# Kernel tuning notes

Hardware: AMD Instinct MI355X
Metric: run time of the kernel (lower is better)

## Reference

```python
import jax, jax.numpy as jnp
import numpy as np

N, K, D = 50000, 16, 128
EPS = 1e-5

def _linear_params(key, fan_in, shape_w, shape_b):
    k1, k2 = jax.random.split(key)
    s = 1.0 / np.sqrt(fan_in)
    W = jax.random.uniform(k1, shape_w, minval=-s, maxval=s, dtype=jnp.float32)
    b = jax.random.uniform(k2, shape_b, minval=-s, maxval=s, dtype=jnp.float32)
    return W, b

def setup_inputs() -> dict:
    key = jax.random.key(0)
    ks = jax.random.split(key, 9)
    Wh, bh = _linear_params(ks[0], D, (D, D), (D,))
    Wt, bt = _linear_params(ks[1], D, (D, D), (D,))
    W1, b1 = _linear_params(ks[2], D, (D, D), (D,))
    W2, b2 = _linear_params(ks[3], D, (D, D), (D,))
    return {
        "x": jax.random.normal(ks[4], (N, D), dtype=jnp.float32),
        "e_h_input": jax.random.normal(ks[5], (N, D), dtype=jnp.float32),
        "e_t_input": jax.random.normal(ks[6], (N, D), dtype=jnp.float32),
        "topk_indices": jax.random.randint(ks[7], (N, K), 0, N),
        "topk_weights": jax.random.uniform(ks[8], (N, K), dtype=jnp.float32),
        "Wh": Wh, "bh": bh, "Wt": Wt, "bt": bt,
        "W1": W1, "b1": b1, "W2": W2, "b2": b2,
        "gamma": jnp.ones((D,), jnp.float32),
        "beta": jnp.zeros((D,), jnp.float32),
    }

def reference(x, e_h_input, e_t_input, topk_indices, topk_weights,
              Wh, bh, Wt, bt, W1, b1, W2, b2, gamma, beta):
    e_h = e_h_input @ Wh.T + bh            # [N, D]
    e_t = e_t_input @ Wt.T + bt            # [N, D]
    Nb_h = e_t[topk_indices]               # [N, K, D] neighbor gather
    p = topk_weights[..., None]            # [N, K, 1]
    e_h_exp = e_h[:, None, :]              # [N, 1, D]
    eh_r = p * Nb_h + (1.0 - p) * e_h_exp  # gated mix
    gate = jnp.tanh(e_h_exp + eh_r)
    ka_prob = jax.nn.softmax(jnp.sum(Nb_h * gate, axis=-1), axis=-1)  # [N, K]
    e_Nh = jnp.einsum('nk,nkd->nd', ka_prob, Nb_h)                    # [N, D]
    sum_emb = jax.nn.leaky_relu((x + e_Nh) @ W1.T + b1, 0.01)
    bi_emb = jax.nn.leaky_relu((x * e_Nh) @ W2.T + b2, 0.01)
    h = sum_emb + bi_emb                   # dropout is identity in eval
    mu = jnp.mean(h, axis=-1, keepdims=True)
    var = jnp.var(h, axis=-1, keepdims=True)
    return (h - mu) / jnp.sqrt(var + EPS) * gamma + beta
```

## Files before the change

kernel.cpp:

```cpp
#include <hip/hip_runtime.h>
#include <stdint.h>

#define NROWS 50000
#define KNB 16
#define DD 128
#define LN_EPS 1e-5f

typedef unsigned short ushort_t;
using frag_ab = __attribute__((ext_vector_type(8))) short;
using frag_cd = __attribute__((ext_vector_type(4))) float;

static __device__ __forceinline__ float bf2f(uint32_t u) {
    union { uint32_t i; float f; } v; v.i = u << 16; return v.f;
}
static __device__ __forceinline__ ushort_t f2bf(float f) {
    union { float f; uint32_t i; } v; v.f = f;
    uint32_t x = v.i;
    return (ushort_t)((x + 0x7fffu + ((x >> 16) & 1u)) >> 16);
}
static __device__ __forceinline__ float leaky(float v) {
    return v > 0.0f ? v : 0.01f * v;
}
static __device__ __forceinline__ float tanh_fast(float z) {
    float e = __expf(2.0f * z);
    return 1.0f - 2.0f / (e + 1.0f);
}
static __device__ __forceinline__ void split_bf(float f, ushort_t& hi, ushort_t& lo) {
    hi = f2bf(f);
    lo = f2bf(f - bf2f(hi));
}
static __device__ __forceinline__ uint32_t cvtpk(float lo, float hi) {
    uint32_t r;
    asm("v_cvt_pk_bf16_f32 %0, %1, %2" : "=v"(r) : "v"(lo), "v"(hi));
    return r;
}
static __device__ __forceinline__ frag_ab load_wfrag(const float* wp) {
    float4 u = *(const float4*)(wp);
    float4 v = *(const float4*)(wp + 4);
    union { uint32_t d[4]; frag_ab f; } r;
    r.d[0] = cvtpk(u.x, u.y);
    r.d[1] = cvtpk(u.z, u.w);
    r.d[2] = cvtpk(v.x, v.y);
    r.d[3] = cvtpk(v.z, v.w);
    return r.f;
}

__global__ __launch_bounds__(256, 4) void linear_stream(
    const float* __restrict__ inA, const float* __restrict__ WA,
    const float* __restrict__ bA, float* __restrict__ outA,
    const float* __restrict__ inB, const float* __restrict__ WB,
    const float* __restrict__ bB, float* __restrict__ outB, int half)
{
    const int which = blockIdx.x >= half;
    const int bid   = which ? blockIdx.x - half : blockIdx.x;
    const float* in   = which ? inB : inA;
    const float* W    = which ? WB  : WA;
    const float* bias = which ? bB  : bA;
    float* out        = which ? outB : outA;

    const int tid  = threadIdx.x;
    const int wv   = tid >> 6;
    const int lane = tid & 63;
    const int quad = lane >> 4, lq = lane & 15;
    const int n0   = wv * 32;

    frag_ab BW[2][4];
    #pragma unroll
    for (int t = 0; t < 2; ++t) {
        const float* wr = W + (size_t)(n0 + t * 16 + lq) * DD + quad * 8;
        #pragma unroll
        for (int kc = 0; kc < 4; ++kc)
            BW[t][kc] = load_wfrag(wr + kc * 32);
    }
    float bn[2];
    #pragma unroll
    for (int t = 0; t < 2; ++t) bn[t] = bias[n0 + t * 16 + lq];

    const int ntiles = NROWS / 16;
    for (int t0 = bid; t0 < ntiles; t0 += half) {
        const int r0 = t0 * 16;
        frag_ab Ahi[4], Alo[4];
        const float* ip = in + (size_t)(r0 + lq) * DD + quad * 8;
        #pragma unroll
        for (int kc = 0; kc < 4; ++kc) {
            float4 u = *(const float4*)(ip + kc * 32);
            float4 v = *(const float4*)(ip + kc * 32 + 4);
            float uu[8] = {u.x, u.y, u.z, u.w, v.x, v.y, v.z, v.w};
            #pragma unroll
            for (int i = 0; i < 8; ++i) {
                ushort_t h, l; split_bf(uu[i], h, l);
                Ahi[kc][i] = (short)h; Alo[kc][i] = (short)l;
            }
        }
        #pragma unroll
        for (int t = 0; t < 2; ++t) {
            frag_cd acc = {0.f, 0.f, 0.f, 0.f};
            #pragma unroll
            for (int kc = 0; kc < 4; ++kc) {
                acc = __builtin_amdgcn_mfma_f32_16x16x32_bf16(Alo[kc], BW[t][kc], acc, 0, 0, 0);
                acc = __builtin_amdgcn_mfma_f32_16x16x32_bf16(Ahi[kc], BW[t][kc], acc, 0, 0, 0);
            }
            #pragma unroll
            for (int r = 0; r < 4; ++r)
                out[(size_t)(r0 + quad * 4 + r) * DD + n0 + t * 16 + lq] = acc[r] + bn[t];
        }
    }
}

__global__ __launch_bounds__(256, 4) void mega_kernel(
    const float* e_h, const float* __restrict__ e_t,
    const int* __restrict__ topk_idx, const float* __restrict__ topk_w,
    const float* __restrict__ x,
    const float* W1, const float* __restrict__ b1,
    const float* W2, const float* __restrict__ b2,
    const float* __restrict__ gamma, const float* __restrict__ beta,
    float* out, int niters)
{
    __shared__ ushort_t aHi[16][136], aLo[16][136];
    __shared__ ushort_t mHi[16][136], mLo[16][136];
    __shared__ float hL[16][132];

    const int tid  = threadIdx.x;
    const int wv   = tid >> 6;
    const int lane = tid & 63;
    const int quad = lane >> 4, lq = lane & 15;
    const int n0   = wv * 32;

    float b1v[2], b2v[2];
    #pragma unroll
    for (int t = 0; t < 2; ++t) {
        b1v[t] = b1[n0 + t * 16 + lq];
        b2v[t] = b2[n0 + t * 16 + lq];
    }
    const float g0 = gamma[lane], g1 = gamma[lane + 64];
    const float be0 = beta[lane], be1 = beta[lane + 64];

    const float* w1p = W1 + (size_t)(n0 + lq) * DD + quad * 8;
    const float* w2p = W2 + (size_t)(n0 + lq) * DD + quad * 8;

    for (int c = blockIdx.x; c < niters; c += gridDim.x) {
        const int r0 = c << 4;

        #pragma unroll
        for (int q = 0; q < 4; ++q) {
            const int lr = 4 * wv + q;
            const int nu = __builtin_amdgcn_readfirstlane(r0 + lr);
            int   tk[KNB];
            float pk[KNB];
            #pragma unroll
            for (int k = 0; k < KNB; ++k) tk[k] = topk_idx[nu * KNB + k];
            #pragma unroll
            for (int k = 0; k < KNB; ++k) pk[k] = topk_w[nu * KNB + k];
            float2 nb[KNB];
            #pragma unroll
            for (int k = 0; k < KNB; ++k) {
                int t = tk[k];
                t = ((unsigned)t < (unsigned)NROWS) ? t : 0;
                nb[k] = *(const float2*)(e_t + (size_t)t * DD + 2 * lane);
            }
            const float2 ehv = *(const float2*)(e_h + (size_t)nu * DD + 2 * lane);
            const float2 xv  = *(const float2*)(x   + (size_t)nu * DD + 2 * lane);

            const float e2x = ehv.x + ehv.x, e2y = ehv.y + ehv.y;

            float s[KNB];
            #pragma unroll
            for (int k = 0; k < KNB; ++k) {
                const float p = pk[k];
                const float ax = __builtin_fmaf(p, nb[k].x - ehv.x, e2x);
                const float ay = __builtin_fmaf(p, nb[k].y - ehv.y, e2y);
                float part = nb[k].x * tanh_fast(ax)
                           + nb[k].y * tanh_fast(ay);
                #pragma unroll
                for (int off = 32; off >= 1; off >>= 1)
                    part += __shfl_xor(part, off, 64);
                s[k] = part;
            }
            float mx = s[0];
            #pragma unroll
            for (int k = 1; k < KNB; ++k) mx = fmaxf(mx, s[k]);
            float sum = 0.0f;
            #pragma unroll
            for (int k = 0; k < KNB; ++k) { s[k] = __expf(s[k] - mx); sum += s[k]; }
            const float inv = 1.0f / sum;
            float e0 = 0.0f, e1 = 0.0f;
            #pragma unroll
            for (int k = 0; k < KNB; ++k) { e0 += s[k] * nb[k].x; e1 += s[k] * nb[k].y; }
            e0 *= inv; e1 *= inv;

            const float a0 = xv.x + e0, a1 = xv.y + e1;
            const float m0 = xv.x * e0, m1 = xv.y * e1;
            ushort_t h0, l0, h1, l1;
            split_bf(a0, h0, l0); split_bf(a1, h1, l1);
            *(uint32_t*)(&aHi[lr][2 * lane]) = (uint32_t)h0 | ((uint32_t)h1 << 16);
            *(uint32_t*)(&aLo[lr][2 * lane]) = (uint32_t)l0 | ((uint32_t)l1 << 16);
            split_bf(m0, h0, l0); split_bf(m1, h1, l1);
            *(uint32_t*)(&mHi[lr][2 * lane]) = (uint32_t)h0 | ((uint32_t)h1 << 16);
            *(uint32_t*)(&mLo[lr][2 * lane]) = (uint32_t)l0 | ((uint32_t)l1 << 16);
        }
        __syncthreads();

        {
            frag_cd aA0 = {0.f,0.f,0.f,0.f}, aA1 = {0.f,0.f,0.f,0.f};
            frag_cd aM0 = {0.f,0.f,0.f,0.f}, aM1 = {0.f,0.f,0.f,0.f};
            #pragma unroll
            for (int kc = 0; kc < 4; ++kc) {
                frag_ab B10 = load_wfrag(w1p + kc * 32);
                frag_ab B11 = load_wfrag(w1p + 16 * DD + kc * 32);
                frag_ab B20 = load_wfrag(w2p + kc * 32);
                frag_ab B21 = load_wfrag(w2p + 16 * DD + kc * 32);
                frag_ab Ah = *(const frag_ab*)(&aHi[lq][kc * 32 + quad * 8]);
                frag_ab Al = *(const frag_ab*)(&aLo[lq][kc * 32 + quad * 8]);
                frag_ab Mh = *(const frag_ab*)(&mHi[lq][kc * 32 + quad * 8]);
                frag_ab Ml = *(const frag_ab*)(&mLo[lq][kc * 32 + quad * 8]);
                aA0 = __builtin_amdgcn_mfma_f32_16x16x32_bf16(Al, B10, aA0, 0, 0, 0);
                aA0 = __builtin_amdgcn_mfma_f32_16x16x32_bf16(Ah, B10, aA0, 0, 0, 0);
                aA1 = __builtin_amdgcn_mfma_f32_16x16x32_bf16(Al, B11, aA1, 0, 0, 0);
                aA1 = __builtin_amdgcn_mfma_f32_16x16x32_bf16(Ah, B11, aA1, 0, 0, 0);
                aM0 = __builtin_amdgcn_mfma_f32_16x16x32_bf16(Ml, B20, aM0, 0, 0, 0);
                aM0 = __builtin_amdgcn_mfma_f32_16x16x32_bf16(Mh, B20, aM0, 0, 0, 0);
                aM1 = __builtin_amdgcn_mfma_f32_16x16x32_bf16(Ml, B21, aM1, 0, 0, 0);
                aM1 = __builtin_amdgcn_mfma_f32_16x16x32_bf16(Mh, B21, aM1, 0, 0, 0);
            }
            #pragma unroll
            for (int r = 0; r < 4; ++r) {
                const int row = quad * 4 + r;
                hL[row][n0 + lq]      = leaky(aA0[r] + b1v[0]) + leaky(aM0[r] + b2v[0]);
                hL[row][n0 + 16 + lq] = leaky(aA1[r] + b1v[1]) + leaky(aM1[r] + b2v[1]);
            }
        }
        __syncthreads();

        #pragma unroll
        for (int q = 0; q < 4; ++q) {
            const int lr = 4 * wv + q;
            const float h0 = hL[lr][lane], h1 = hL[lr][lane + 64];
            float s = h0 + h1, qq = h0 * h0 + h1 * h1;
            #pragma unroll
            for (int off = 32; off >= 1; off >>= 1) {
                s  += __shfl_xor(s,  off, 64);
                qq += __shfl_xor(qq, off, 64);
            }
            const float mu  = s * (1.0f / DD);
            const float var = qq * (1.0f / DD) - mu * mu;
            const float rs  = rsqrtf(var + LN_EPS);
            out[(size_t)(r0 + lr) * DD + lane]      = (h0 - mu) * rs * g0 + be0;
            out[(size_t)(r0 + lr) * DD + lane + 64] = (h1 - mu) * rs * g1 + be1;
        }
        __syncthreads();
    }
}

extern "C" void kernel_launch(void* const* d_in, const int* in_sizes, int n_in,
                              void* d_out, int out_size, void* d_ws, size_t ws_size,
                              hipStream_t stream) {
    const float* x      = (const float*)d_in[0];
    const float* ehi    = (const float*)d_in[1];
    const float* eti    = (const float*)d_in[2];
    const int*   tidx   = (const int*)d_in[3];
    const float* tw     = (const float*)d_in[4];
    const float* Wh     = (const float*)d_in[5];
    const float* bh     = (const float*)d_in[6];
    const float* Wt     = (const float*)d_in[7];
    const float* bt     = (const float*)d_in[8];
    const float* W1     = (const float*)d_in[9];
    const float* b1     = (const float*)d_in[10];
    const float* W2     = (const float*)d_in[11];
    const float* b2     = (const float*)d_in[12];
    const float* gamma  = (const float*)d_in[13];
    const float* beta   = (const float*)d_in[14];

    float* e_h = (float*)d_out;
    float* e_t = (float*)d_ws;

    const int half = 1024;
    linear_stream<<<2 * half, 256, 0, stream>>>(ehi, Wh, bh, e_h,
                                                eti, Wt, bt, e_t, half);
    mega_kernel<<<1536, 256, 0, stream>>>(e_h, e_t, tidx, tw, x,
                                          W1, b1, W2, b2, gamma, beta,
                                          (float*)d_out, NROWS / 16);
}
```

Before: 306.6 us.

## Fuse e_h projection into mega kernel, computing it per tile into LDS

The Wh linear projection moves out of the separate streaming kernel and into the main kernel. Each 16-row tile computes e_h with split-bf16 MFMAs and stores it in shared memory, so the 25.6MB e_h intermediate is never written to or read back from global memory. The first kernel now handles only e_t, and the main kernel grid shrinks from 1536 to 1024 blocks. In exchange, the main kernel reloads and converts Wh fragments from global memory every tile, needs more LDS, and adds a __syncthreads, which may reduce occupancy.

After: 309.5 us. About the same (+0.9%).

```diff
diff --git a/kernel.cpp b/kernel.cpp
--- a/kernel.cpp
+++ b/kernel.cpp
@@ -44,20 +44,21 @@
     r.d[3] = cvtpk(v.z, v.w);
     return r.f;
 }
+static __device__ __forceinline__ void load_afrag(const float* ip, frag_ab& hi, frag_ab& lo) {
+    float4 u = *(const float4*)(ip);
+    float4 v = *(const float4*)(ip + 4);
+    float uu[8] = {u.x, u.y, u.z, u.w, v.x, v.y, v.z, v.w};
+    #pragma unroll
+    for (int i = 0; i < 8; ++i) {
+        ushort_t h, l; split_bf(uu[i], h, l);
+        hi[i] = (short)h; lo[i] = (short)l;
+    }
+}
 
 __global__ __launch_bounds__(256, 4) void linear_stream(
-    const float* __restrict__ inA, const float* __restrict__ WA,
-    const float* __restrict__ bA, float* __restrict__ outA,
-    const float* __restrict__ inB, const float* __restrict__ WB,
-    const float* __restrict__ bB, float* __restrict__ outB, int half)
+    const float* __restrict__ in, const float* __restrict__ W,
+    const float* __restrict__ bias, float* __restrict__ out)
 {
-    const int which = blockIdx.x >= half;
-    const int bid   = which ? blockIdx.x - half : blockIdx.x;
-    const float* in   = which ? inB : inA;
-    const float* W    = which ? WB  : WA;
-    const float* bias = which ? bB  : bA;
-    float* out        = which ? outB : outA;
-
     const int tid  = threadIdx.x;
     const int wv   = tid >> 6;
     const int lane = tid & 63;
@@ -77,21 +78,13 @@
     for (int t = 0; t < 2; ++t) bn[t] = bias[n0 + t * 16 + lq];
 
     const int ntiles = NROWS / 16;
-    for (int t0 = bid; t0 < ntiles; t0 += half) {
+    for (int t0 = blockIdx.x; t0 < ntiles; t0 += gridDim.x) {
         const int r0 = t0 * 16;
         frag_ab Ahi[4], Alo[4];
         const float* ip = in + (size_t)(r0 + lq) * DD + quad * 8;
         #pragma unroll
-        for (int kc = 0; kc < 4; ++kc) {
-            float4 u = *(const float4*)(ip + kc * 32);
-            float4 v = *(const float4*)(ip + kc * 32 + 4);
-            float uu[8] = {u.x, u.y, u.z, u.w, v.x, v.y, v.z, v.w};
-            #pragma unroll
-            for (int i = 0; i < 8; ++i) {
-                ushort_t h, l; split_bf(uu[i], h, l);
-                Ahi[kc][i] = (short)h; Alo[kc][i] = (short)l;
-            }
-        }
+        for (int kc = 0; kc < 4; ++kc)
+            load_afrag(ip + kc * 32, Ahi[kc], Alo[kc]);
         #pragma unroll
         for (int t = 0; t < 2; ++t) {
             frag_cd acc = {0.f, 0.f, 0.f, 0.f};
@@ -108,7 +101,8 @@
 }
 
 __global__ __launch_bounds__(256, 4) void mega_kernel(
-    const float* e_h, const float* __restrict__ e_t,
+    const float* __restrict__ ehi, const float* Wh, const float* __restrict__ bh,
+    const float* __restrict__ e_t,
     const int* __restrict__ topk_idx, const float* __restrict__ topk_w,
     const float* __restrict__ x,
     const float* W1, const float* __restrict__ b1,
@@ -119,6 +113,7 @@
     __shared__ ushort_t aHi[16][136], aLo[16][136];
     __shared__ ushort_t mHi[16][136], mLo[16][136];
     __shared__ float hL[16][132];
+    __shared__ float ehL[16][132];
 
     const int tid  = threadIdx.x;
     const int wv   = tid >> 6;
@@ -126,20 +121,44 @@
     const int quad = lane >> 4, lq = lane & 15;
     const int n0   = wv * 32;
 
-    float b1v[2], b2v[2];
+    float b1v[2], b2v[2], bhv[2];
     #pragma unroll
     for (int t = 0; t < 2; ++t) {
         b1v[t] = b1[n0 + t * 16 + lq];
         b2v[t] = b2[n0 + t * 16 + lq];
+        bhv[t] = bh[n0 + t * 16 + lq];
     }
     const float g0 = gamma[lane], g1 = gamma[lane + 64];
     const float be0 = beta[lane], be1 = beta[lane + 64];
 
     const float* w1p = W1 + (size_t)(n0 + lq) * DD + quad * 8;
     const float* w2p = W2 + (size_t)(n0 + lq) * DD + quad * 8;
+    const float* whp = Wh + (size_t)(n0 + lq) * DD + quad * 8;
 
     for (int c = blockIdx.x; c < niters; c += gridDim.x) {
         const int r0 = c << 4;
+
+        {
+            frag_ab Ehi[4], Elo[4];
+            const float* ip = ehi + (size_t)(r0 + lq) * DD + quad * 8;
+            #pragma unroll
+            for (int kc = 0; kc < 4; ++kc)
+                load_afrag(ip + kc * 32, Ehi[kc], Elo[kc]);
+            #pragma unroll
+            for (int t = 0; t < 2; ++t) {
+                frag_cd acc = {0.f, 0.f, 0.f, 0.f};
+                #pragma unroll
+                for (int kc = 0; kc < 4; ++kc) {
+                    frag_ab Bh = load_wfrag(whp + t * 16 * DD + kc * 32);
+                    acc = __builtin_amdgcn_mfma_f32_16x16x32_bf16(Elo[kc], Bh, acc, 0, 0, 0);
+                    acc = __builtin_amdgcn_mfma_f32_16x16x32_bf16(Ehi[kc], Bh, acc, 0, 0, 0);
+                }
+                #pragma unroll
+                for (int r = 0; r < 4; ++r)
+                    ehL[quad * 4 + r][n0 + t * 16 + lq] = acc[r] + bhv[t];
+            }
+        }
+        __syncthreads();
 
         #pragma unroll
         for (int q = 0; q < 4; ++q) {
@@ -158,8 +177,8 @@
                 t = ((unsigned)t < (unsigned)NROWS) ? t : 0;
                 nb[k] = *(const float2*)(e_t + (size_t)t * DD + 2 * lane);
             }
-            const float2 ehv = *(const float2*)(e_h + (size_t)nu * DD + 2 * lane);
-            const float2 xv  = *(const float2*)(x   + (size_t)nu * DD + 2 * lane);
+            const float2 ehv = *(const float2*)(&ehL[lr][2 * lane]);
+            const float2 xv  = *(const float2*)(x + (size_t)nu * DD + 2 * lane);
 
             const float e2x = ehv.x + ehv.x, e2y = ehv.y + ehv.y;
 
@@ -270,13 +289,10 @@
     const float* gamma  = (const float*)d_in[13];
     const float* beta   = (const float*)d_in[14];
 
-    float* e_h = (float*)d_out;
     float* e_t = (float*)d_ws;
 
-    const int half = 1024;
-    linear_stream<<<2 * half, 256, 0, stream>>>(ehi, Wh, bh, e_h,
-                                                eti, Wt, bt, e_t, half);
-    mega_kernel<<<1536, 256, 0, stream>>>(e_h, e_t, tidx, tw, x,
+    linear_stream<<<1024, 256, 0, stream>>>(eti, Wt, bt, e_t);
+    mega_kernel<<<1024, 256, 0, stream>>>(ehi, Wh, bh, e_t, tidx, tw, x,
                                           W1, b1, W2, b2, gamma, beta,
                                           (float*)d_out, NROWS / 16);
 }
```

## Split LayerNorm out of fused kernel into separate in-place pass

Applied to the files above, without the earlier changes.

The fused kernel now writes the pre-norm activations straight to the output buffer. It drops the shared hL staging tile and the second per-tile barrier. A new ln_kernel then reads each row back, does the mean/variance shuffle reduction and rewrites the normalized row in place. The fused kernel's grid also shrinks from 1536 to 1024 blocks. This lowers LDS use and sync pressure in the main kernel, at the cost of an extra full read and write of the output and one more kernel launch.

Result: faster. 297.1 us (-3.1%).

```diff
diff --git a/kernel.cpp b/kernel.cpp
--- a/kernel.cpp
+++ b/kernel.cpp
@@ -43,6 +43,16 @@
     r.d[2] = cvtpk(v.x, v.y);
     r.d[3] = cvtpk(v.z, v.w);
     return r.f;
+}
+static __device__ __forceinline__ void load_afrag(const float* ip, frag_ab& hi, frag_ab& lo) {
+    float4 u = *(const float4*)(ip);
+    float4 v = *(const float4*)(ip + 4);
+    float uu[8] = {u.x, u.y, u.z, u.w, v.x, v.y, v.z, v.w};
+    #pragma unroll
+    for (int i = 0; i < 8; ++i) {
+        ushort_t h, l; split_bf(uu[i], h, l);
+        hi[i] = (short)h; lo[i] = (short)l;
+    }
 }
 
 __global__ __launch_bounds__(256, 4) void linear_stream(
@@ -82,16 +92,8 @@
         frag_ab Ahi[4], Alo[4];
         const float* ip = in + (size_t)(r0 + lq) * DD + quad * 8;
         #pragma unroll
-        for (int kc = 0; kc < 4; ++kc) {
-            float4 u = *(const float4*)(ip + kc * 32);
-            float4 v = *(const float4*)(ip + kc * 32 + 4);
-            float uu[8] = {u.x, u.y, u.z, u.w, v.x, v.y, v.z, v.w};
-            #pragma unroll
-            for (int i = 0; i < 8; ++i) {
-                ushort_t h, l; split_bf(uu[i], h, l);
-                Ahi[kc][i] = (short)h; Alo[kc][i] = (short)l;
-            }
-        }
+        for (int kc = 0; kc < 4; ++kc)
+            load_afrag(ip + kc * 32, Ahi[kc], Alo[kc]);
         #pragma unroll
         for (int t = 0; t < 2; ++t) {
             frag_cd acc = {0.f, 0.f, 0.f, 0.f};
@@ -113,12 +115,10 @@
     const float* __restrict__ x,
     const float* W1, const float* __restrict__ b1,
     const float* W2, const float* __restrict__ b2,
-    const float* __restrict__ gamma, const float* __restrict__ beta,
     float* out, int niters)
 {
     __shared__ ushort_t aHi[16][136], aLo[16][136];
     __shared__ ushort_t mHi[16][136], mLo[16][136];
-    __shared__ float hL[16][132];
 
     const int tid  = threadIdx.x;
     const int wv   = tid >> 6;
@@ -132,8 +132,6 @@
         b1v[t] = b1[n0 + t * 16 + lq];
         b2v[t] = b2[n0 + t * 16 + lq];
     }
-    const float g0 = gamma[lane], g1 = gamma[lane + 64];
-    const float be0 = beta[lane], be1 = beta[lane + 64];
 
     const float* w1p = W1 + (size_t)(n0 + lq) * DD + quad * 8;
     const float* w2p = W2 + (size_t)(n0 + lq) * DD + quad * 8;
@@ -224,30 +222,37 @@
             }
             #pragma unroll
             for (int r = 0; r < 4; ++r) {
-                const int row = quad * 4 + r;
-                hL[row][n0 + lq]      = leaky(aA0[r] + b1v[0]) + leaky(aM0[r] + b2v[0]);
-                hL[row][n0 + 16 + lq] = leaky(aA1[r] + b1v[1]) + leaky(aM1[r] + b2v[1]);
+                const size_t gr = (size_t)(r0 + quad * 4 + r) * DD;
+                out[gr + n0 + lq]      = leaky(aA0[r] + b1v[0]) + leaky(aM0[r] + b2v[0]);
+                out[gr + n0 + 16 + lq] = leaky(aA1[r] + b1v[1]) + leaky(aM1[r] + b2v[1]);
             }
         }
         __syncthreads();
-
-        #pragma unroll
-        for (int q = 0; q < 4; ++q) {
-            const int lr = 4 * wv + q;
-            const float h0 = hL[lr][lane], h1 = hL[lr][lane + 64];
-            float s = h0 + h1, qq = h0 * h0 + h1 * h1;
-            #pragma unroll
-            for (int off = 32; off >= 1; off >>= 1) {
-                s  += __shfl_xor(s,  off, 64);
-                qq += __shfl_xor(qq, off, 64);
-            }
-            const float mu  = s * (1.0f / DD);
-            const float var = qq * (1.0f / DD) - mu * mu;
-            const float rs  = rsqrtf(var + LN_EPS);
-            out[(size_t)(r0 + lr) * DD + lane]      = (h0 - mu) * rs * g0 + be0;
-            out[(size_t)(r0 + lr) * DD + lane + 64] = (h1 - mu) * rs * g1 + be1;
-        }
-        __syncthreads();
+    }
+}
+
+__global__ __launch_bounds__(256) void ln_kernel(
+    float* out, const float* __restrict__ gamma, const float* __restrict__ beta)
+{
+    const int wv   = threadIdx.x >> 6;
+    const int lane = threadIdx.x & 63;
+    const float g0 = gamma[lane], g1 = gamma[lane + 64];
+    const float be0 = beta[lane], be1 = beta[lane + 64];
+
+    for (int r = blockIdx.x * 4 + wv; r < NROWS; r += gridDim.x * 4) {
+        float* rp = out + (size_t)r * DD;
+        const float h0 = rp[lane], h1 = rp[lane + 64];
+        float s = h0 + h1, qq = h0 * h0 + h1 * h1;
+        #pragma unroll
+        for (int off = 32; off >= 1; off >>= 1) {
+            s  += __shfl_xor(s,  off, 64);
+            qq += __shfl_xor(qq, off, 64);
+        }
+        const float mu  = s * (1.0f / DD);
+        const float var = qq * (1.0f / DD) - mu * mu;
+        const float rs  = rsqrtf(var + LN_EPS);
+        rp[lane]      = (h0 - mu) * rs * g0 + be0;
+        rp[lane + 64] = (h1 - mu) * rs * g1 + be1;
     }
 }
 
@@ -276,7 +281,8 @@
     const int half = 1024;
     linear_stream<<<2 * half, 256, 0, stream>>>(ehi, Wh, bh, e_h,
                                                 eti, Wt, bt, e_t, half);
-    mega_kernel<<<1536, 256, 0, stream>>>(e_h, e_t, tidx, tw, x,
-                                          W1, b1, W2, b2, gamma, beta,
+    mega_kernel<<<1024, 256, 0, stream>>>(e_h, e_t, tidx, tw, x,
+                                          W1, b1, W2, b2,
                                           (float*)d_out, NROWS / 16);
-}
+    ln_kernel<<<2048, 256, 0, stream>>>((float*)d_out, gamma, beta);
+}
```
